# Kernel optimization log

Measured on AMD Instinct MI355X. Metric: run time of the kernel, lower is better.

Reference implementation:

```python
import jax, jax.numpy as jnp
import numpy as np

N_NODES = 100000
N_EDGES = 1200000
NEG_SLOPE = 0.2
EPS = 1e-16


def _glorot(key, shape):
    fan_in, fan_out = shape[0], shape[-1]
    lim = float(np.sqrt(6.0 / (fan_in + fan_out)))
    return jax.random.uniform(key, shape, jnp.float32, -lim, lim)


def setup_inputs() -> dict:
    key = jax.random.key(0)
    ks = jax.random.split(key, 16)
    x = jax.random.normal(ks[0], (N_NODES, 3), jnp.float32)
    edge_index = jax.random.randint(ks[1], (2, N_EDGES), 0, N_NODES, jnp.int64)
    # conv1: in=3 -> heads=4, ch=64
    W1 = _glorot(ks[2], (3, 256));   a_src1 = _glorot(ks[3], (4, 64));  a_dst1 = _glorot(ks[4], (4, 64));  b1 = jnp.zeros((256,), jnp.float32)
    # conv2: in=256 -> heads=4, ch=64
    W2 = _glorot(ks[5], (256, 256)); a_src2 = _glorot(ks[6], (4, 64));  a_dst2 = _glorot(ks[7], (4, 64));  b2 = jnp.zeros((256,), jnp.float32)
    # conv3: in=256 -> heads=1, ch=32, concat=False (mean over heads)
    W3 = _glorot(ks[8], (256, 32));  a_src3 = _glorot(ks[9], (1, 32));  a_dst3 = _glorot(ks[10], (1, 32)); b3 = jnp.zeros((32,), jnp.float32)
    return dict(x=x, edge_index=edge_index,
                W1=W1, a_src1=a_src1, a_dst1=a_dst1, b1=b1,
                W2=W2, a_src2=a_src2, a_dst2=a_dst2, b2=b2,
                W3=W3, a_src3=a_src3, a_dst3=a_dst3, b3=b3)


def gat_conv(x, src, dst, W, a_src, a_dst, b, concat):
    """PyG-style GATConv (shared lin, per-dst segment softmax)."""
    N = x.shape[0]
    H, C = a_src.shape
    h = (x @ W).reshape(N, H, C)                           # [N,H,C]
    as_n = jnp.einsum('nhc,hc->nh', h, a_src)              # [N,H]
    ad_n = jnp.einsum('nhc,hc->nh', h, a_dst)              # [N,H]
    alpha = jax.nn.leaky_relu(as_n[src] + ad_n[dst], NEG_SLOPE)  # [E,H]
    m = jax.ops.segment_max(alpha, dst, num_segments=N)    # per-dst max for stability
    e = jnp.exp(alpha - m[dst])
    s = jax.ops.segment_sum(e, dst, num_segments=N)
    w = e / (s[dst] + EPS)                                 # [E,H] normalized attention
    out = jax.ops.segment_sum(h[src] * w[:, :, None], dst, num_segments=N)  # [N,H,C]
    out = out.reshape(N, H * C) if concat else out.mean(axis=1)
    return out + b


def reference(x, edge_index, W1, a_src1, a_dst1, b1, W2, a_src2, a_dst2, b2, W3, a_src3, a_dst3, b3):
    N = x.shape[0]
    loop = jnp.arange(N, dtype=edge_index.dtype)
    src = jnp.concatenate([edge_index[0], loop])           # add_self_loops=True
    dst = jnp.concatenate([edge_index[1], loop])
    h = jax.nn.relu(gat_conv(x, src, dst, W1, a_src1, a_dst1, b1, concat=True))
    # dropout p=0.2 is identity in eval mode
    h = jax.nn.relu(gat_conv(h, src, dst, W2, a_src2, a_dst2, b2, concat=True))
    out = gat_conv(h, src, dst, W3, a_src3, a_dst3, b3, concat=False)
    return out
```

## Files before the change

### kernel.cpp

```cpp
#include <hip/hip_runtime.h>


#define NEG_SLOPE 0.2f
#define SM_EPS 1e-16f
#define SCAN_CHUNK 2048

typedef __bf16 bf16x8 __attribute__((ext_vector_type(8)));
typedef float f32x4 __attribute__((ext_vector_type(4)));
typedef unsigned int u32x4 __attribute__((ext_vector_type(4)));

__device__ __forceinline__ float bf2f(unsigned short u) {
  union { unsigned int i; float f; } v; v.i = ((unsigned int)u) << 16; return v.f;
}
__device__ __forceinline__ unsigned short f2bf(float f) {
  union { float f; unsigned int i; } v; v.f = f;
  unsigned int lsb = (v.i >> 16) & 1u;
  v.i += 0x7fffu + lsb;
  return (unsigned short)(v.i >> 16);
}
__device__ __forceinline__ void bf2x(unsigned int u, float& f0, float& f1) {
  union { unsigned int i; float f; } a, b;
  a.i = u << 16; b.i = u & 0xffff0000u;
  f0 = a.f; f1 = b.f;
}

__global__ void detect_i64_kernel(const int* __restrict__ ei, int* __restrict__ flag) {
  if (blockIdx.x == 0 && threadIdx.x == 0) {
    int orv = 0;
    for (int k = 0; k < 64; ++k) orv |= ei[2 * k + 1];
    *flag = (orv == 0) ? 1 : 0;
  }
}

__device__ __forceinline__ int load_idx(const int* __restrict__ ei, int logical, int is64) {
  return is64 ? ei[2 * logical] : ei[logical];
}

__global__ void deg_pos_kernel(const int* __restrict__ ei, int E,
                               const int* __restrict__ flag,
                               int* __restrict__ cnt, int* __restrict__ pos) {
  int i = blockIdx.x * blockDim.x + threadIdx.x;
  if (i < E) {
    int d = load_idx(ei, E + i, *flag);
    pos[i] = atomicAdd(&cnt[d], 1);
  }
}

__global__ __launch_bounds__(256) void scan_phaseA(const int* __restrict__ deg,
                                                   int* __restrict__ bsum, int N) {
  int t = threadIdx.x;
  int base = blockIdx.x * SCAN_CHUNK + t * 8;
  int s = 0;
#pragma unroll
  for (int i = 0; i < 8; ++i) {
    int idx = base + i;
    if (idx < N) s += deg[idx] + 1;
  }
  __shared__ int red[256];
  red[t] = s;
  __syncthreads();
  for (int d = 128; d > 0; d >>= 1) {
    if (t < d) red[t] += red[t + d];
    __syncthreads();
  }
  if (t == 0) bsum[blockIdx.x] = red[0];
}

__global__ __launch_bounds__(256) void scan_phaseC(const int* __restrict__ deg,
                                                   const int* __restrict__ bsum,
                                                   int* __restrict__ rowptr, int N) {
  int t = threadIdx.x;
  __shared__ int blkoff;
  if (t == 0) {
    int o = 0;
    for (int i = 0; i < (int)blockIdx.x; ++i) o += bsum[i];
    blkoff = o;
  }
  int base = blockIdx.x * SCAN_CHUNK + t * 8;
  int v[8];
  int s = 0;
#pragma unroll
  for (int i = 0; i < 8; ++i) {
    int idx = base + i;
    v[i] = (idx < N) ? deg[idx] + 1 : 0;
    s += v[i];
  }
  __shared__ int sh[256];
  sh[t] = s;
  __syncthreads();
  for (int d = 1; d < 256; d <<= 1) {
    int u = (t >= d) ? sh[t - d] : 0;
    __syncthreads();
    sh[t] += u;
    __syncthreads();
  }
  int run = blkoff + sh[t] - s;
#pragma unroll
  for (int i = 0; i < 8; ++i) {
    int idx = base + i;
    if (idx < N) rowptr[idx] = run;
    run += v[i];
  }
  if (base < N && base + 8 >= N) rowptr[N] = run;
}

__global__ void scatter2_kernel(const int* __restrict__ ei, int E, int N,
                                const int* __restrict__ flag,
                                const int* __restrict__ rowptr,
                                const int* __restrict__ pos, int* __restrict__ colA) {
  int i = blockIdx.x * blockDim.x + threadIdx.x;
  int is64 = *flag;
  if (i < E) {
    int s = load_idx(ei, i, is64);
    int d = load_idx(ei, E + i, is64);
    __builtin_nontemporal_store(s, &colA[rowptr[d] + pos[i]]);
  } else if (i < E + N) {
    int n = i - E;
    __builtin_nontemporal_store(n, &colA[rowptr[n + 1] - 1]);
  }
}

__global__ void wt_bf16_both(const float* __restrict__ W2, const float* __restrict__ W3,
                             unsigned short* __restrict__ w2t, unsigned short* __restrict__ w3t) {
  int idx = blockIdx.x * 256 + threadIdx.x;
  if (idx < 256 * 256) {
    int k = idx >> 8, n = idx & 255;
    w2t[(size_t)n * 256 + k] = f2bf(W2[idx]);
  } else {
    int j = idx - 256 * 256;
    if (j < 256 * 32) {
      int k = j >> 5, n = j & 31;
      w3t[(size_t)n * 256 + k] = f2bf(W3[j]);
    }
  }
}

__global__ __launch_bounds__(256) void prep_small(
    const float* __restrict__ W1, const float* __restrict__ as1, const float* __restrict__ ad1,
    const float* __restrict__ W2, const float* __restrict__ as2, const float* __restrict__ ad2,
    float* __restrict__ A1s, float* __restrict__ A1d,
    float* __restrict__ A2s, float* __restrict__ A2d) {
  int c = threadIdx.x;
#pragma unroll
  for (int h = 0; h < 4; ++h) {
    float vs = 0.f, vd = 0.f;
    const float* wrow = W2 + (size_t)c * 256 + h * 64;
    const float* s2 = as2 + h * 64;
    const float* d2 = ad2 + h * 64;
    for (int cc = 0; cc < 64; ++cc) {
      float w = wrow[cc];
      vs += w * s2[cc];
      vd += w * d2[cc];
    }
    A2s[c * 4 + h] = vs;
    A2d[c * 4 + h] = vd;
  }
  if (c < 3) {
#pragma unroll
    for (int h = 0; h < 4; ++h) {
      float vs = 0.f, vd = 0.f;
      const float* wrow = W1 + (size_t)c * 256 + h * 64;
      const float* s1 = as1 + h * 64;
      const float* d1 = ad1 + h * 64;
      for (int cc = 0; cc < 64; ++cc) {
        float w = wrow[cc];
        vs += w * s1[cc];
        vd += w * d1[cc];
      }
      A1s[c * 4 + h] = vs;
      A1d[c * 4 + h] = vd;
    }
  }
}

__global__ __launch_bounds__(256) void k1_asv1(const float* __restrict__ x,
                                               const float* __restrict__ A1s,
                                               const float* __restrict__ A1d,
                                               float* __restrict__ asv, float* __restrict__ adv,
                                               int N) {
  int n = blockIdx.x * 256 + threadIdx.x;
  if (n >= N) return;
  float x0 = x[n * 3 + 0], x1 = x[n * 3 + 1], x2 = x[n * 3 + 2];
  f32x4 s, d;
#pragma unroll
  for (int h = 0; h < 4; ++h) {
    s[h] = x0 * A1s[h] + x1 * A1s[4 + h] + x2 * A1s[8 + h];
    d[h] = x0 * A1d[h] + x1 * A1d[4 + h] + x2 * A1d[8 + h];
  }
  *(f32x4*)(asv + (size_t)n * 4) = s;
  *(f32x4*)(adv + (size_t)n * 4) = d;
}

__global__ __launch_bounds__(256) void k2_aggx(
    const float* __restrict__ x, const float* __restrict__ asv,
    const float* __restrict__ adv, const int* __restrict__ rowptr,
    const int* __restrict__ colA, float* __restrict__ agg, int N) {
  int wv = threadIdx.x >> 6;
  int d = blockIdx.x * 4 + wv;
  if (d >= N) return;
  int lane = threadIdx.x & 63;
  int h4 = lane >> 4, el = lane & 15;
  int r0 = rowptr[d], r1 = rowptr[d + 1];
  int len = r1 - r0;
  float ad = adv[(size_t)d * 4 + h4];
  float m = -1e30f, s = 0.f;
  float ax = 0.f, ay = 0.f, az = 0.f;
  for (int base = 0; base < len; base += 16) {
    int rem = len - base; if (rem > 16) rem = 16;
    int sc = 0;
    float alpha = -1e30f;
    if (el < rem) {
      sc = colA[r0 + base + el];
      float a = asv[(size_t)sc * 4 + h4] + ad;
      alpha = (a > 0.f) ? a : NEG_SLOPE * a;
    }
    float mx = alpha;
#pragma unroll
    for (int off = 1; off < 16; off <<= 1) mx = fmaxf(mx, __shfl_xor(mx, off));
    float mn = fmaxf(m, mx);
    float scale = __expf(m - mn);
    float w = (el < rem) ? __expf(alpha - mn) : 0.f;
    float cs = w;
#pragma unroll
    for (int off = 1; off < 16; off <<= 1) cs += __shfl_xor(cs, off);
    s = s * scale + cs;
    m = mn;
    ax *= scale; ay *= scale; az *= scale;
    if (el < rem) {
      ax += w * x[(size_t)sc * 3 + 0];
      ay += w * x[(size_t)sc * 3 + 1];
      az += w * x[(size_t)sc * 3 + 2];
    }
  }
#pragma unroll
  for (int off = 1; off < 16; off <<= 1) {
    ax += __shfl_xor(ax, off);
    ay += __shfl_xor(ay, off);
    az += __shfl_xor(az, off);
  }
  if (el == 0) {
    float inv = 1.f / (s + SM_EPS);
    agg[(size_t)d * 12 + h4 * 3 + 0] = ax * inv;
    agg[(size_t)d * 12 + h4 * 3 + 1] = ay * inv;
    agg[(size_t)d * 12 + h4 * 3 + 2] = az * inv;
  }
}

__global__ __launch_bounds__(256) void k3_expand(
    const float* __restrict__ agg, const float* __restrict__ W1,
    const float* __restrict__ b1, const float* __restrict__ A2s,
    const float* __restrict__ A2d, unsigned short* __restrict__ h,
    float* __restrict__ asv, float* __restrict__ adv, int N) {
  int wv = threadIdx.x >> 6, lane = threadIdx.x & 63;
  int n = blockIdx.x * 4 + wv;
  if (n >= N) return;
  int hb = lane >> 4;
  float a0 = agg[(size_t)n * 12 + hb * 3 + 0];
  float a1 = agg[(size_t)n * 12 + hb * 3 + 1];
  float a2 = agg[(size_t)n * 12 + hb * 3 + 2];
  float vs[4] = {}, vd[4] = {};
  unsigned short o[4];
#pragma unroll
  for (int j = 0; j < 4; ++j) {
    int c = lane * 4 + j;
    float val = a0 * W1[c] + a1 * W1[256 + c] + a2 * W1[512 + c] + b1[c];
    val = fmaxf(val, 0.f);
    o[j] = f2bf(val);
#pragma unroll
    for (int h2 = 0; h2 < 4; ++h2) {
      vs[h2] += val * A2s[c * 4 + h2];
      vd[h2] += val * A2d[c * 4 + h2];
    }
  }
  *(uint2*)(h + (size_t)n * 256 + lane * 4) = *(uint2*)o;
#pragma unroll
  for (int off = 1; off < 64; off <<= 1) {
#pragma unroll
    for (int h2 = 0; h2 < 4; ++h2) {
      vs[h2] += __shfl_xor(vs[h2], off);
      vd[h2] += __shfl_xor(vd[h2], off);
    }
  }
  if (lane == 0) {
    f32x4 s, d;
#pragma unroll
    for (int h2 = 0; h2 < 4; ++h2) { s[h2] = vs[h2]; d[h2] = vd[h2]; }
    *(f32x4*)(asv + (size_t)n * 4) = s;
    *(f32x4*)(adv + (size_t)n * 4) = d;
  }
}

__global__ __launch_bounds__(256) void gemm_mfma_w256(
    const unsigned short* __restrict__ A, const unsigned short* __restrict__ Bt,
    unsigned short* __restrict__ C, int M, int K) {
  constexpr int BM = 64, BK = 64;
  __shared__ unsigned short As[BM][BK + 8];
  __shared__ unsigned short Bs[256][BK + 8];
  const int bm = blockIdx.x * BM;
  const int tid = threadIdx.x, wid = tid >> 6, lane = tid & 63;
  const int lrow = lane & 15, lkh = lane >> 4;
  const int srow = tid >> 3, scol = (tid & 7) * 8;
  f32x4 acc[4][4] = {};
  for (int k0 = 0; k0 < K; k0 += BK) {
#pragma unroll
    for (int r0 = 0; r0 < BM; r0 += 32) {
      int r = r0 + srow, gr = bm + r;
      uint4 v = make_uint4(0u, 0u, 0u, 0u);
      if (gr < M) v = *(const uint4*)(A + (size_t)gr * K + k0 + scol);
      *(uint4*)(&As[r][scol]) = v;
    }
#pragma unroll
    for (int r0 = 0; r0 < 256; r0 += 32) {
      int r = r0 + srow;
      uint4 v = *(const uint4*)(Bt + (size_t)r * K + k0 + scol);
      *(uint4*)(&Bs[r][scol]) = v;
    }
    __syncthreads();
#pragma unroll
    for (int kk = 0; kk < 2; ++kk) {
      bf16x8 a[4], b[4];
#pragma unroll
      for (int m = 0; m < 4; ++m)
        a[m] = *(const bf16x8*)(&As[m * 16 + lrow][kk * 32 + lkh * 8]);
#pragma unroll
      for (int n = 0; n < 4; ++n)
        b[n] = *(const bf16x8*)(&Bs[wid * 64 + n * 16 + lrow][kk * 32 + lkh * 8]);
#pragma unroll
      for (int m = 0; m < 4; ++m)
#pragma unroll
        for (int n = 0; n < 4; ++n)
          acc[m][n] = __builtin_amdgcn_mfma_f32_16x16x32_bf16(a[m], b[n], acc[m][n], 0, 0, 0);
    }
    __syncthreads();
  }
#pragma unroll
  for (int m = 0; m < 4; ++m) {
#pragma unroll
    for (int q = 0; q < 4; ++q) {
      int grow = bm + m * 16 + lkh * 4 + q;
      if (grow < M) {
#pragma unroll
        for (int n = 0; n < 4; ++n)
          C[(size_t)grow * 256 + wid * 64 + n * 16 + lrow] = f2bf(acc[m][n][q]);
      }
    }
  }
}

template <int WR, int WC, int ATT_H>
__global__ __launch_bounds__(64 * WR * WC) void gemm_mfma(
    const unsigned short* __restrict__ A, const unsigned short* __restrict__ Bt,
    unsigned short* __restrict__ C, const float* __restrict__ a_src,
    const float* __restrict__ a_dst, float* __restrict__ asv, float* __restrict__ adv,
    int M, int N, int K) {
  constexpr int BM = 32 * WR, BN = 32 * WC, BK = 64;
  constexpr int T = 64 * WR * WC;
  constexpr int RPP = T / 8;
  __shared__ unsigned short As[BM][BK + 8];
  __shared__ unsigned short Bs[BN][BK + 8];
  const int bm = blockIdx.y * BM, bn = blockIdx.x * BN;
  const int tid = threadIdx.x, wid = tid >> 6, lane = tid & 63;
  const int wr = wid / WC, wc = wid % WC;
  const int lrow = lane & 15, lkh = lane >> 4;
  const int srow = tid >> 3, scol = (tid & 7) * 8;
  f32x4 acc[2][2] = {};
  for (int k0 = 0; k0 < K; k0 += BK) {
#pragma unroll
    for (int r0 = 0; r0 < BM; r0 += RPP) {
      int r = r0 + srow, gr = bm + r;
      uint4 v = make_uint4(0u, 0u, 0u, 0u);
      if (gr < M) v = *(const uint4*)(A + (size_t)gr * K + k0 + scol);
      *(uint4*)(&As[r][scol]) = v;
    }
#pragma unroll
    for (int r0 = 0; r0 < BN; r0 += RPP) {
      int r = r0 + srow;
      if (r < BN) {
        int gn = bn + r;
        uint4 v = *(const uint4*)(Bt + (size_t)gn * K + k0 + scol);
        *(uint4*)(&Bs[r][scol]) = v;
      }
    }
    __syncthreads();
#pragma unroll
    for (int kk = 0; kk < 2; ++kk) {
      bf16x8 a0 = *(const bf16x8*)(&As[wr * 32 + lrow][kk * 32 + lkh * 8]);
      bf16x8 a1 = *(const bf16x8*)(&As[wr * 32 + 16 + lrow][kk * 32 + lkh * 8]);
      bf16x8 b0 = *(const bf16x8*)(&Bs[wc * 32 + lrow][kk * 32 + lkh * 8]);
      bf16x8 b1 = *(const bf16x8*)(&Bs[wc * 32 + 16 + lrow][kk * 32 + lkh * 8]);
      acc[0][0] = __builtin_amdgcn_mfma_f32_16x16x32_bf16(a0, b0, acc[0][0], 0, 0, 0);
      acc[0][1] = __builtin_amdgcn_mfma_f32_16x16x32_bf16(a0, b1, acc[0][1], 0, 0, 0);
      acc[1][0] = __builtin_amdgcn_mfma_f32_16x16x32_bf16(a1, b0, acc[1][0], 0, 0, 0);
      acc[1][1] = __builtin_amdgcn_mfma_f32_16x16x32_bf16(a1, b1, acc[1][1], 0, 0, 0);
    }
    __syncthreads();
  }
#pragma unroll
  for (int m = 0; m < 2; ++m) {
#pragma unroll
    for (int q = 0; q < 4; ++q) {
      int grow = bm + wr * 32 + m * 16 + lkh * 4 + q;
      if (grow < M) {
#pragma unroll
        for (int n = 0; n < 2; ++n) {
          int gcol = bn + wc * 32 + n * 16 + lrow;
          C[(size_t)grow * N + gcol] = f2bf(acc[m][n][q]);
        }
      }
    }
  }
  const int hh = (ATT_H == 1) ? 0 : (int)blockIdx.x;
  float asl[2], adl[2];
#pragma unroll
  for (int n = 0; n < 2; ++n) {
    int c = wc * 32 + n * 16 + lrow;
    asl[n] = a_src[hh * BN + c];
    adl[n] = a_dst[hh * BN + c];
  }
#pragma unroll
  for (int m = 0; m < 2; ++m) {
#pragma unroll
    for (int q = 0; q < 4; ++q) {
      float ps = acc[m][0][q] * asl[0] + acc[m][1][q] * asl[1];
      float pd = acc[m][0][q] * adl[0] + acc[m][1][q] * adl[1];
#pragma unroll
      for (int off = 1; off < 16; off <<= 1) {
        ps += __shfl_xor(ps, off);
        pd += __shfl_xor(pd, off);
      }
      int grow = bm + wr * 32 + m * 16 + lkh * 4 + q;
      if (lrow == 0 && grow < M) {
        asv[(size_t)grow * ATT_H + hh] = ps;
        adv[(size_t)grow * ATT_H + hh] = pd;
      }
    }
  }
}

template <bool RELU>
__global__ __launch_bounds__(256) void gat_fused256(
    const unsigned short* __restrict__ hbuf, const float* __restrict__ asv,
    const float* __restrict__ adv, const int* __restrict__ rowptr,
    const int* __restrict__ colA, const float* __restrict__ bias,
    unsigned short* __restrict__ outb, int N) {
  int wv = threadIdx.x >> 6;
  int d = blockIdx.x * 4 + wv;
  if (d >= N) return;
  int lane = threadIdx.x & 63;
  int h4 = lane >> 4, el = lane & 15;
  int g = lane >> 5, c32 = lane & 31;
  int hh = c32 >> 3;
  int r0 = rowptr[d], r1 = rowptr[d + 1];
  int len = r1 - r0;
  float ad = adv[(size_t)d * 4 + h4];
  float m = -1e30f, s = 0.f;
  float acc[8] = {};
  const int hsrc = hh * 16;
  for (int base = 0; base < len; base += 16) {
    int rem = len - base; if (rem > 16) rem = 16;
    int sc = 0;
    float alpha = -1e30f;
    if (el < rem) {
      sc = colA[r0 + base + el];
      float a = asv[(size_t)sc * 4 + h4] + ad;
      alpha = (a > 0.f) ? a : NEG_SLOPE * a;
    }
    float mx = alpha;
#pragma unroll
    for (int off = 1; off < 16; off <<= 1) mx = fmaxf(mx, __shfl_xor(mx, off));
    float mn = fmaxf(m, mx);
    float scale = __expf(m - mn);
    float w = (el < rem) ? __expf(alpha - mn) : 0.f;
    float cs = w;
#pragma unroll
    for (int off = 1; off < 16; off <<= 1) cs += __shfl_xor(cs, off);
    s = s * scale + cs;
    m = mn;
    float scale_h = __shfl(scale, hsrc);
#pragma unroll
    for (int j = 0; j < 8; ++j) acc[j] *= scale_h;
    int e2 = 0;
    for (; e2 + 4 <= rem; e2 += 4) {
      int ea = e2 + g, eb = e2 + 2 + g;
      float wa = __shfl(w, hsrc + ea);
      int sa = __shfl(sc, hsrc + ea);
      float wb = __shfl(w, hsrc + eb);
      int sb = __shfl(sc, hsrc + eb);
      uint4 hva = *(const uint4*)(hbuf + (size_t)sa * 256 + c32 * 8);
      uint4 hvb = *(const uint4*)(hbuf + (size_t)sb * 256 + c32 * 8);
      float f0, f1;
      bf2x(hva.x, f0, f1); acc[0] += wa * f0; acc[1] += wa * f1;
      bf2x(hva.y, f0, f1); acc[2] += wa * f0; acc[3] += wa * f1;
      bf2x(hva.z, f0, f1); acc[4] += wa * f0; acc[5] += wa * f1;
      bf2x(hva.w, f0, f1); acc[6] += wa * f0; acc[7] += wa * f1;
      bf2x(hvb.x, f0, f1); acc[0] += wb * f0; acc[1] += wb * f1;
      bf2x(hvb.y, f0, f1); acc[2] += wb * f0; acc[3] += wb * f1;
      bf2x(hvb.z, f0, f1); acc[4] += wb * f0; acc[5] += wb * f1;
      bf2x(hvb.w, f0, f1); acc[6] += wb * f0; acc[7] += wb * f1;
    }
    for (; e2 < rem; e2 += 2) {
      int e = e2 + g;
      float w_e = __shfl(w, hsrc + (e & 15));
      int sc_e = __shfl(sc, hsrc + (e & 15));
      uint4 hv = *(const uint4*)(hbuf + (size_t)sc_e * 256 + c32 * 8);
      float f0, f1;
      bf2x(hv.x, f0, f1); acc[0] += w_e * f0; acc[1] += w_e * f1;
      bf2x(hv.y, f0, f1); acc[2] += w_e * f0; acc[3] += w_e * f1;
      bf2x(hv.z, f0, f1); acc[4] += w_e * f0; acc[5] += w_e * f1;
      bf2x(hv.w, f0, f1); acc[6] += w_e * f0; acc[7] += w_e * f1;
    }
  }
#pragma unroll
  for (int j = 0; j < 8; ++j) acc[j] += __shfl_xor(acc[j], 32);
  float inv = 1.f / (__shfl(s, hsrc) + SM_EPS);
  if (g == 0) {
    unsigned short o[8];
#pragma unroll
    for (int j = 0; j < 8; ++j) {
      float v = acc[j] * inv + bias[c32 * 8 + j];
      if (RELU) v = fmaxf(v, 0.f);
      o[j] = f2bf(v);
    }
    __builtin_nontemporal_store(*(u32x4*)o, (u32x4*)(outb + (size_t)d * 256 + c32 * 8));
  }
}

__global__ __launch_bounds__(256) void gat_fused32(
    const unsigned short* __restrict__ hbuf, const float* __restrict__ asv,
    const float* __restrict__ adv, const int* __restrict__ rowptr,
    const int* __restrict__ colA, const float* __restrict__ bias,
    float* __restrict__ out, int N) {
  int wv = threadIdx.x >> 6;
  int d = blockIdx.x * 4 + wv;
  if (d >= N) return;
  int lane = threadIdx.x & 63;
  int slot = lane >> 3, ci = lane & 7;
  int r0 = rowptr[d], r1 = rowptr[d + 1];
  int len = r1 - r0;
  float ad = adv[d];
  float m = -1e30f, s = 0.f;
  float a0 = 0.f, a1 = 0.f, a2 = 0.f, a3 = 0.f;
  for (int base = 0; base < len; base += 64) {
    int rem = len - base; if (rem > 64) rem = 64;
    int sc = 0;
    float alpha = -1e30f;
    if (lane < rem) {
      sc = colA[r0 + base + lane];
      float a = asv[sc] + ad;
      alpha = (a > 0.f) ? a : NEG_SLOPE * a;
    }
    float mx = alpha;
#pragma unroll
    for (int off = 1; off < 64; off <<= 1) mx = fmaxf(mx, __shfl_xor(mx, off));
    float mn = fmaxf(m, mx);
    float scale = __expf(m - mn);
    float w = (lane < rem) ? __expf(alpha - mn) : 0.f;
    float cs = w;
#pragma unroll
    for (int off = 1; off < 64; off <<= 1) cs += __shfl_xor(cs, off);
    s = s * scale + cs;
    m = mn;
    a0 *= scale; a1 *= scale; a2 *= scale; a3 *= scale;
    for (int e2 = 0; e2 < rem; e2 += 8) {
      int e = e2 + slot;
      float w_e = __shfl(w, e);
      int sc_e = __shfl(sc, e);
      uint2 hv = *(const uint2*)(hbuf + (size_t)sc_e * 32 + ci * 4);
      float f0, f1;
      bf2x(hv.x, f0, f1); a0 += w_e * f0; a1 += w_e * f1;
      bf2x(hv.y, f0, f1); a2 += w_e * f0; a3 += w_e * f1;
    }
  }
#pragma unroll
  for (int off = 8; off < 64; off <<= 1) {
    a0 += __shfl_xor(a0, off);
    a1 += __shfl_xor(a1, off);
    a2 += __shfl_xor(a2, off);
    a3 += __shfl_xor(a3, off);
  }
  if (slot == 0) {
    float inv = 1.f / (s + SM_EPS);
    f32x4 o;
    o.x = a0 * inv + bias[ci * 4 + 0];
    o.y = a1 * inv + bias[ci * 4 + 1];
    o.z = a2 * inv + bias[ci * 4 + 2];
    o.w = a3 * inv + bias[ci * 4 + 3];
    __builtin_nontemporal_store(o, (f32x4*)(out + (size_t)d * 32 + ci * 4));
  }
}

extern "C" void kernel_launch(void* const* d_in, const int* in_sizes, int n_in,
                              void* d_out, int out_size, void* d_ws, size_t ws_size,
                              hipStream_t stream) {
  const float* x   = (const float*)d_in[0];
  const int*   ei  = (const int*)d_in[1];
  const float* W1  = (const float*)d_in[2];
  const float* as1 = (const float*)d_in[3];
  const float* ad1 = (const float*)d_in[4];
  const float* b1  = (const float*)d_in[5];
  const float* W2  = (const float*)d_in[6];
  const float* as2 = (const float*)d_in[7];
  const float* ad2 = (const float*)d_in[8];
  const float* b2  = (const float*)d_in[9];
  const float* W3  = (const float*)d_in[10];
  const float* as3 = (const float*)d_in[11];
  const float* ad3 = (const float*)d_in[12];
  const float* b3  = (const float*)d_in[13];
  float* out = (float*)d_out;

  const int N = in_sizes[0] / 3;
  const int E = in_sizes[1] / 2;
  const int ET = E + N;

  char* ws = (char*)d_ws;
  size_t off = 0;
  auto alloc = [&](size_t bytes) -> void* {
    void* p = ws + off;
    off = (off + bytes + 255) & ~(size_t)255;
    return p;
  };
  unsigned short* bufA = (unsigned short*)alloc((size_t)N * 256 * 2);
  unsigned short* bufB = (unsigned short*)alloc((size_t)N * 256 * 2);
  unsigned short* w2t  = (unsigned short*)alloc((size_t)256 * 256 * 2);
  unsigned short* w3t  = (unsigned short*)alloc((size_t)32 * 256 * 2);
  float* asbuf  = (float*)alloc((size_t)N * 4 * 4);
  float* adbuf  = (float*)alloc((size_t)N * 4 * 4);
  float* aggbuf = (float*)alloc((size_t)N * 12 * 4);
  int*   rowptr = (int*)alloc((size_t)(N + 1) * 4);
  int*   cnt    = (int*)alloc((size_t)N * 4);
  int*   posb   = (int*)alloc((size_t)E * 4);
  int*   colA   = (int*)alloc((size_t)ET * 4);
  int*   bsum   = (int*)alloc(1024);
  int*   dflag  = (int*)alloc(256);
  float* A1s    = (float*)alloc(12 * 4);
  float* A1d    = (float*)alloc(12 * 4);
  float* A2s    = (float*)alloc(1024 * 4);
  float* A2d    = (float*)alloc(1024 * 4);
  (void)ws_size;

  const int nScanB = (N + SCAN_CHUNK - 1) / SCAN_CHUNK;

  detect_i64_kernel<<<1, 64, 0, stream>>>(ei, dflag);
  hipMemsetAsync(cnt, 0, (size_t)N * 4, stream);
  prep_small<<<1, 256, 0, stream>>>(W1, as1, ad1, W2, as2, ad2, A1s, A1d, A2s, A2d);
  wt_bf16_both<<<(256 * 256 + 256 * 32 + 255) / 256, 256, 0, stream>>>(W2, W3, w2t, w3t);
  deg_pos_kernel<<<(E + 255) / 256, 256, 0, stream>>>(ei, E, dflag, cnt, posb);
  scan_phaseA<<<nScanB, 256, 0, stream>>>(cnt, bsum, N);
  scan_phaseC<<<nScanB, 256, 0, stream>>>(cnt, bsum, rowptr, N);
  scatter2_kernel<<<(ET + 255) / 256, 256, 0, stream>>>(ei, E, N, dflag, rowptr, posb, colA);

  const int nb4 = (N + 3) / 4;

  k1_asv1<<<(N + 255) / 256, 256, 0, stream>>>(x, A1s, A1d, asbuf, adbuf, N);
  k2_aggx<<<nb4, 256, 0, stream>>>(x, asbuf, adbuf, rowptr, colA, aggbuf, N);
  k3_expand<<<nb4, 256, 0, stream>>>(aggbuf, W1, b1, A2s, A2d, bufB, asbuf, adbuf, N);

  gemm_mfma_w256<<<(N + 63) / 64, 256, 0, stream>>>(bufB, w2t, bufA, N, 256);
  gat_fused256<true><<<nb4, 256, 0, stream>>>(bufA, asbuf, adbuf, rowptr, colA, b2, bufB, N);

  {
    dim3 grid(1, (N + 127) / 128);
    gemm_mfma<4, 1, 1><<<grid, 256, 0, stream>>>(bufB, w3t, bufA, as3, ad3, asbuf, adbuf,
                                                 N, 32, 256);
  }
  gat_fused32<<<nb4, 256, 0, stream>>>(bufA, asbuf, adbuf, rowptr, colA, b3, out, N);
}
```

Before: 430.3 us.

## Merge prep kernels into one launch, fuse layer-1 aggregation with expansion, widen GEMM tile

Combines degree counting, layer-1 attention projection, weight transpose/convert and A2 precompute into a single block-dispatched kernel, which removes several launches. Fuses the layer-1 softmax aggregation with the 3->256 expansion so the intermediate agg buffer is no longer written and re-read. Separate as/ad buffers are added so the fused kernel does not overwrite the layer-1 scores other waves are still reading. Doubles the layer-2 GEMM block to 128 rows with 512 threads so each B tile load in shared memory is reused across more rows, at the cost of larger blocks and lower occupancy.

Result: faster. 400.1 us (-7.0%).

```diff
diff --git a/kernel.cpp b/kernel.cpp
--- a/kernel.cpp
+++ b/kernel.cpp
@@ -36,13 +36,78 @@
   return is64 ? ei[2 * logical] : ei[logical];
 }
 
-__global__ void deg_pos_kernel(const int* __restrict__ ei, int E,
-                               const int* __restrict__ flag,
-                               int* __restrict__ cnt, int* __restrict__ pos) {
-  int i = blockIdx.x * blockDim.x + threadIdx.x;
-  if (i < E) {
-    int d = load_idx(ei, E + i, *flag);
-    pos[i] = atomicAdd(&cnt[d], 1);
+__global__ __launch_bounds__(256) void prep_mega(
+    const int* __restrict__ ei, int E, const int* __restrict__ flag,
+    int* __restrict__ cnt, int* __restrict__ pos,
+    const float* __restrict__ x, const float* __restrict__ W1,
+    const float* __restrict__ as1, const float* __restrict__ ad1,
+    float* __restrict__ asv, float* __restrict__ adv, int N,
+    const float* __restrict__ W2, const float* __restrict__ W3,
+    unsigned short* __restrict__ w2t, unsigned short* __restrict__ w3t,
+    const float* __restrict__ as2, const float* __restrict__ ad2,
+    float* __restrict__ A2s, float* __restrict__ A2d,
+    int nbDeg, int nbK1, int nbWt) {
+  int bid = blockIdx.x;
+  int t = threadIdx.x;
+  if (bid < nbDeg) {
+    int i = bid * 256 + t;
+    if (i < E) {
+      int d = load_idx(ei, E + i, *flag);
+      pos[i] = atomicAdd(&cnt[d], 1);
+    }
+  } else if (bid < nbDeg + nbK1) {
+    __shared__ float A1[24];
+    if (t < 24) {
+      int e = t % 12;
+      int k = e >> 2, h = e & 3;
+      const float* av = (t < 12) ? as1 : ad1;
+      const float* wr = W1 + k * 256 + h * 64;
+      const float* a = av + h * 64;
+      float v = 0.f;
+      for (int c = 0; c < 64; ++c) v += wr[c] * a[c];
+      A1[t] = v;
+    }
+    __syncthreads();
+    int n = (bid - nbDeg) * 256 + t;
+    if (n < N) {
+      float x0 = x[n * 3 + 0], x1 = x[n * 3 + 1], x2 = x[n * 3 + 2];
+      f32x4 s, d;
+#pragma unroll
+      for (int h = 0; h < 4; ++h) {
+        s[h] = x0 * A1[h] + x1 * A1[4 + h] + x2 * A1[8 + h];
+        d[h] = x0 * A1[12 + h] + x1 * A1[16 + h] + x2 * A1[20 + h];
+      }
+      *(f32x4*)(asv + (size_t)n * 4) = s;
+      *(f32x4*)(adv + (size_t)n * 4) = d;
+    }
+  } else if (bid < nbDeg + nbK1 + nbWt) {
+    int idx = (bid - nbDeg - nbK1) * 256 + t;
+    if (idx < 256 * 256) {
+      int k = idx >> 8, n = idx & 255;
+      w2t[(size_t)n * 256 + k] = f2bf(W2[idx]);
+    } else {
+      int j = idx - 256 * 256;
+      if (j < 256 * 32) {
+        int k = j >> 5, n = j & 31;
+        w3t[(size_t)n * 256 + k] = f2bf(W3[j]);
+      }
+    }
+  } else {
+    int c = t;
+#pragma unroll
+    for (int h = 0; h < 4; ++h) {
+      float vs = 0.f, vd = 0.f;
+      const float* wrow = W2 + (size_t)c * 256 + h * 64;
+      const float* s2 = as2 + h * 64;
+      const float* d2 = ad2 + h * 64;
+      for (int cc = 0; cc < 64; ++cc) {
+        float w = wrow[cc];
+        vs += w * s2[cc];
+        vd += w * d2[cc];
+      }
+      A2s[c * 4 + h] = vs;
+      A2d[c * 4 + h] = vd;
+    }
   }
 }
 
@@ -120,81 +185,13 @@
   }
 }
 
-__global__ void wt_bf16_both(const float* __restrict__ W2, const float* __restrict__ W3,
-                             unsigned short* __restrict__ w2t, unsigned short* __restrict__ w3t) {
-  int idx = blockIdx.x * 256 + threadIdx.x;
-  if (idx < 256 * 256) {
-    int k = idx >> 8, n = idx & 255;
-    w2t[(size_t)n * 256 + k] = f2bf(W2[idx]);
-  } else {
-    int j = idx - 256 * 256;
-    if (j < 256 * 32) {
-      int k = j >> 5, n = j & 31;
-      w3t[(size_t)n * 256 + k] = f2bf(W3[j]);
-    }
-  }
-}
-
-__global__ __launch_bounds__(256) void prep_small(
-    const float* __restrict__ W1, const float* __restrict__ as1, const float* __restrict__ ad1,
-    const float* __restrict__ W2, const float* __restrict__ as2, const float* __restrict__ ad2,
-    float* __restrict__ A1s, float* __restrict__ A1d,
-    float* __restrict__ A2s, float* __restrict__ A2d) {
-  int c = threadIdx.x;
-#pragma unroll
-  for (int h = 0; h < 4; ++h) {
-    float vs = 0.f, vd = 0.f;
-    const float* wrow = W2 + (size_t)c * 256 + h * 64;
-    const float* s2 = as2 + h * 64;
-    const float* d2 = ad2 + h * 64;
-    for (int cc = 0; cc < 64; ++cc) {
-      float w = wrow[cc];
-      vs += w * s2[cc];
-      vd += w * d2[cc];
-    }
-    A2s[c * 4 + h] = vs;
-    A2d[c * 4 + h] = vd;
-  }
-  if (c < 3) {
-#pragma unroll
-    for (int h = 0; h < 4; ++h) {
-      float vs = 0.f, vd = 0.f;
-      const float* wrow = W1 + (size_t)c * 256 + h * 64;
-      const float* s1 = as1 + h * 64;
-      const float* d1 = ad1 + h * 64;
-      for (int cc = 0; cc < 64; ++cc) {
-        float w = wrow[cc];
-        vs += w * s1[cc];
-        vd += w * d1[cc];
-      }
-      A1s[c * 4 + h] = vs;
-      A1d[c * 4 + h] = vd;
-    }
-  }
-}
-
-__global__ __launch_bounds__(256) void k1_asv1(const float* __restrict__ x,
-                                               const float* __restrict__ A1s,
-                                               const float* __restrict__ A1d,
-                                               float* __restrict__ asv, float* __restrict__ adv,
-                                               int N) {
-  int n = blockIdx.x * 256 + threadIdx.x;
-  if (n >= N) return;
-  float x0 = x[n * 3 + 0], x1 = x[n * 3 + 1], x2 = x[n * 3 + 2];
-  f32x4 s, d;
-#pragma unroll
-  for (int h = 0; h < 4; ++h) {
-    s[h] = x0 * A1s[h] + x1 * A1s[4 + h] + x2 * A1s[8 + h];
-    d[h] = x0 * A1d[h] + x1 * A1d[4 + h] + x2 * A1d[8 + h];
-  }
-  *(f32x4*)(asv + (size_t)n * 4) = s;
-  *(f32x4*)(adv + (size_t)n * 4) = d;
-}
-
-__global__ __launch_bounds__(256) void k2_aggx(
+__global__ __launch_bounds__(256) void k2_fused(
     const float* __restrict__ x, const float* __restrict__ asv,
     const float* __restrict__ adv, const int* __restrict__ rowptr,
-    const int* __restrict__ colA, float* __restrict__ agg, int N) {
+    const int* __restrict__ colA, const float* __restrict__ W1,
+    const float* __restrict__ b1, const float* __restrict__ A2s,
+    const float* __restrict__ A2d, unsigned short* __restrict__ h,
+    float* __restrict__ asv2, float* __restrict__ adv2, int N) {
   int wv = threadIdx.x >> 6;
   int d = blockIdx.x * 4 + wv;
   if (d >= N) return;
@@ -238,32 +235,14 @@
     ay += __shfl_xor(ay, off);
     az += __shfl_xor(az, off);
   }
-  if (el == 0) {
-    float inv = 1.f / (s + SM_EPS);
-    agg[(size_t)d * 12 + h4 * 3 + 0] = ax * inv;
-    agg[(size_t)d * 12 + h4 * 3 + 1] = ay * inv;
-    agg[(size_t)d * 12 + h4 * 3 + 2] = az * inv;
-  }
-}
-
-__global__ __launch_bounds__(256) void k3_expand(
-    const float* __restrict__ agg, const float* __restrict__ W1,
-    const float* __restrict__ b1, const float* __restrict__ A2s,
-    const float* __restrict__ A2d, unsigned short* __restrict__ h,
-    float* __restrict__ asv, float* __restrict__ adv, int N) {
-  int wv = threadIdx.x >> 6, lane = threadIdx.x & 63;
-  int n = blockIdx.x * 4 + wv;
-  if (n >= N) return;
-  int hb = lane >> 4;
-  float a0 = agg[(size_t)n * 12 + hb * 3 + 0];
-  float a1 = agg[(size_t)n * 12 + hb * 3 + 1];
-  float a2 = agg[(size_t)n * 12 + hb * 3 + 2];
+  float inv = 1.f / (s + SM_EPS);
+  ax *= inv; ay *= inv; az *= inv;
   float vs[4] = {}, vd[4] = {};
   unsigned short o[4];
 #pragma unroll
   for (int j = 0; j < 4; ++j) {
     int c = lane * 4 + j;
-    float val = a0 * W1[c] + a1 * W1[256 + c] + a2 * W1[512 + c] + b1[c];
+    float val = ax * W1[c] + ay * W1[256 + c] + az * W1[512 + c] + b1[c];
     val = fmaxf(val, 0.f);
     o[j] = f2bf(val);
 #pragma unroll
@@ -272,7 +251,7 @@
       vd[h2] += val * A2d[c * 4 + h2];
     }
   }
-  *(uint2*)(h + (size_t)n * 256 + lane * 4) = *(uint2*)o;
+  *(uint2*)(h + (size_t)d * 256 + lane * 4) = *(uint2*)o;
 #pragma unroll
   for (int off = 1; off < 64; off <<= 1) {
 #pragma unroll
@@ -282,35 +261,36 @@
     }
   }
   if (lane == 0) {
-    f32x4 s, d;
-#pragma unroll
-    for (int h2 = 0; h2 < 4; ++h2) { s[h2] = vs[h2]; d[h2] = vd[h2]; }
-    *(f32x4*)(asv + (size_t)n * 4) = s;
-    *(f32x4*)(adv + (size_t)n * 4) = d;
-  }
-}
-
-__global__ __launch_bounds__(256) void gemm_mfma_w256(
+    f32x4 sv, dv;
+#pragma unroll
+    for (int h2 = 0; h2 < 4; ++h2) { sv[h2] = vs[h2]; dv[h2] = vd[h2]; }
+    *(f32x4*)(asv2 + (size_t)d * 4) = sv;
+    *(f32x4*)(adv2 + (size_t)d * 4) = dv;
+  }
+}
+
+__global__ __launch_bounds__(512) void gemm_mfma_w256(
     const unsigned short* __restrict__ A, const unsigned short* __restrict__ Bt,
     unsigned short* __restrict__ C, int M, int K) {
-  constexpr int BM = 64, BK = 64;
+  constexpr int BM = 128, BK = 64;
   __shared__ unsigned short As[BM][BK + 8];
   __shared__ unsigned short Bs[256][BK + 8];
   const int bm = blockIdx.x * BM;
   const int tid = threadIdx.x, wid = tid >> 6, lane = tid & 63;
+  const int wr = wid >> 2, wc = wid & 3;
   const int lrow = lane & 15, lkh = lane >> 4;
   const int srow = tid >> 3, scol = (tid & 7) * 8;
   f32x4 acc[4][4] = {};
   for (int k0 = 0; k0 < K; k0 += BK) {
 #pragma unroll
-    for (int r0 = 0; r0 < BM; r0 += 32) {
+    for (int r0 = 0; r0 < BM; r0 += 64) {
       int r = r0 + srow, gr = bm + r;
       uint4 v = make_uint4(0u, 0u, 0u, 0u);
       if (gr < M) v = *(const uint4*)(A + (size_t)gr * K + k0 + scol);
       *(uint4*)(&As[r][scol]) = v;
     }
 #pragma unroll
-    for (int r0 = 0; r0 < 256; r0 += 32) {
+    for (int r0 = 0; r0 < 256; r0 += 64) {
       int r = r0 + srow;
       uint4 v = *(const uint4*)(Bt + (size_t)r * K + k0 + scol);
       *(uint4*)(&Bs[r][scol]) = v;
@@ -321,10 +301,10 @@
       bf16x8 a[4], b[4];
 #pragma unroll
       for (int m = 0; m < 4; ++m)
-        a[m] = *(const bf16x8*)(&As[m * 16 + lrow][kk * 32 + lkh * 8]);
+        a[m] = *(const bf16x8*)(&As[wr * 64 + m * 16 + lrow][kk * 32 + lkh * 8]);
 #pragma unroll
       for (int n = 0; n < 4; ++n)
-        b[n] = *(const bf16x8*)(&Bs[wid * 64 + n * 16 + lrow][kk * 32 + lkh * 8]);
+        b[n] = *(const bf16x8*)(&Bs[wc * 64 + n * 16 + lrow][kk * 32 + lkh * 8]);
 #pragma unroll
       for (int m = 0; m < 4; ++m)
 #pragma unroll
@@ -337,11 +317,11 @@
   for (int m = 0; m < 4; ++m) {
 #pragma unroll
     for (int q = 0; q < 4; ++q) {
-      int grow = bm + m * 16 + lkh * 4 + q;
+      int grow = bm + wr * 64 + m * 16 + lkh * 4 + q;
       if (grow < M) {
 #pragma unroll
         for (int n = 0; n < 4; ++n)
-          C[(size_t)grow * 256 + wid * 64 + n * 16 + lrow] = f2bf(acc[m][n][q]);
+          C[(size_t)grow * 256 + wc * 64 + n * 16 + lrow] = f2bf(acc[m][n][q]);
       }
     }
   }
@@ -625,38 +605,39 @@
   unsigned short* w3t  = (unsigned short*)alloc((size_t)32 * 256 * 2);
   float* asbuf  = (float*)alloc((size_t)N * 4 * 4);
   float* adbuf  = (float*)alloc((size_t)N * 4 * 4);
-  float* aggbuf = (float*)alloc((size_t)N * 12 * 4);
+  float* asbuf2 = (float*)alloc((size_t)N * 4 * 4);
+  float* adbuf2 = (float*)alloc((size_t)N * 4 * 4);
   int*   rowptr = (int*)alloc((size_t)(N + 1) * 4);
   int*   cnt    = (int*)alloc((size_t)N * 4);
   int*   posb   = (int*)alloc((size_t)E * 4);
   int*   colA   = (int*)alloc((size_t)ET * 4);
   int*   bsum   = (int*)alloc(1024);
   int*   dflag  = (int*)alloc(256);
-  float* A1s    = (float*)alloc(12 * 4);
-  float* A1d    = (float*)alloc(12 * 4);
   float* A2s    = (float*)alloc(1024 * 4);
   float* A2d    = (float*)alloc(1024 * 4);
   (void)ws_size;
 
   const int nScanB = (N + SCAN_CHUNK - 1) / SCAN_CHUNK;
+  const int nbDeg = (E + 255) / 256;
+  const int nbK1  = (N + 255) / 256;
+  const int nbWt  = (256 * 256 + 256 * 32 + 255) / 256;
 
   detect_i64_kernel<<<1, 64, 0, stream>>>(ei, dflag);
   hipMemsetAsync(cnt, 0, (size_t)N * 4, stream);
-  prep_small<<<1, 256, 0, stream>>>(W1, as1, ad1, W2, as2, ad2, A1s, A1d, A2s, A2d);
-  wt_bf16_both<<<(256 * 256 + 256 * 32 + 255) / 256, 256, 0, stream>>>(W2, W3, w2t, w3t);
-  deg_pos_kernel<<<(E + 255) / 256, 256, 0, stream>>>(ei, E, dflag, cnt, posb);
+  prep_mega<<<nbDeg + nbK1 + nbWt + 1, 256, 0, stream>>>(
+      ei, E, dflag, cnt, posb, x, W1, as1, ad1, asbuf, adbuf, N,
+      W2, W3, w2t, w3t, as2, ad2, A2s, A2d, nbDeg, nbK1, nbWt);
   scan_phaseA<<<nScanB, 256, 0, stream>>>(cnt, bsum, N);
   scan_phaseC<<<nScanB, 256, 0, stream>>>(cnt, bsum, rowptr, N);
   scatter2_kernel<<<(ET + 255) / 256, 256, 0, stream>>>(ei, E, N, dflag, rowptr, posb, colA);
 
   const int nb4 = (N + 3) / 4;
 
-  k1_asv1<<<(N + 255) / 256, 256, 0, stream>>>(x, A1s, A1d, asbuf, adbuf, N);
-  k2_aggx<<<nb4, 256, 0, stream>>>(x, asbuf, adbuf, rowptr, colA, aggbuf, N);
-  k3_expand<<<nb4, 256, 0, stream>>>(aggbuf, W1, b1, A2s, A2d, bufB, asbuf, adbuf, N);
-
-  gemm_mfma_w256<<<(N + 63) / 64, 256, 0, stream>>>(bufB, w2t, bufA, N, 256);
-  gat_fused256<true><<<nb4, 256, 0, stream>>>(bufA, asbuf, adbuf, rowptr, colA, b2, bufB, N);
+  k2_fused<<<nb4, 256, 0, stream>>>(x, asbuf, adbuf, rowptr, colA, W1, b1,
+                                    A2s, A2d, bufB, asbuf2, adbuf2, N);
+
+  gemm_mfma_w256<<<(N + 127) / 128, 512, 0, stream>>>(bufB, w2t, bufA, N, 256);
+  gat_fused256<true><<<nb4, 256, 0, stream>>>(bufA, asbuf2, adbuf2, rowptr, colA, b2, bufB, N);
 
   {
     dim3 grid(1, (N + 127) / 128);
```
